# Performance work log

Hardware: AMD Instinct MI355X
Metric: run time of the kernel (lower is better)

## Reference

```python
import jax, jax.numpy as jnp
import numpy as np

D_MODEL = 1024
NUM_HEADS = 16
D_K = D_MODEL // NUM_HEADS          # 64
D_ROPE = int(D_K * 0.5)             # 32
ROPE_BASE = 10000.0


def _rope(x):
    # x: [L, B, H, D_K]; rotate first D_ROPE features, pass the rest through.
    L = x.shape[0]
    d = D_ROPE
    theta = 1.0 / (ROPE_BASE ** (jnp.arange(0, d, 2, dtype=jnp.float32) / d))  # [d/2]
    idx_theta = jnp.arange(L, dtype=jnp.float32)[:, None] * theta[None, :]     # [L, d/2]
    idx_theta2 = jnp.concatenate([idx_theta, idx_theta], axis=-1)              # [L, d]
    cos = jnp.cos(idx_theta2)[:, None, None, :].astype(x.dtype)
    sin = jnp.sin(idx_theta2)[:, None, None, :].astype(x.dtype)
    x_rope, x_pass = x[..., :d], x[..., d:]
    neg_half = jnp.concatenate([-x_rope[..., d // 2:], x_rope[..., :d // 2]], axis=-1)
    x_rope = x_rope * cos + neg_half * sin
    return jnp.concatenate([x_rope, x_pass], axis=-1)


def setup_inputs() -> dict:
    key = jax.random.key(0)
    k1, k2 = jax.random.split(key)
    L, B = 2048, 2
    x = jax.random.normal(k1, (L, B, D_MODEL), dtype=jnp.float32)
    # xavier_uniform-like init for in_proj_weight [3*d_model, d_model]
    limit = float(np.sqrt(6.0 / (3 * D_MODEL + D_MODEL)))
    in_proj_weight = jax.random.uniform(k2, (3 * D_MODEL, D_MODEL),
                                        minval=-limit, maxval=limit, dtype=jnp.float32)
    return {"x": x, "in_proj_weight": in_proj_weight}


def reference(x, in_proj_weight):
    L, B, _ = x.shape
    # fused QKV projection: [L, B, 3*d_model]
    qkv = jnp.einsum('ed,lbd->lbe', in_proj_weight, x)
    # NOTE: faithful to original quirk — reshape to per-head blocks of 3*d_k,
    # then chunk along last dim.
    qkv = qkv.reshape(L, B, NUM_HEADS, 3 * D_K)
    q, k, v = qkv[..., :D_K], qkv[..., D_K:2 * D_K], qkv[..., 2 * D_K:]
    q = _rope(q)
    k = _rope(k)
    # [L,B,H,dk] -> [H,B,L,dk]
    q, k, v = (jnp.swapaxes(t, 0, 2) for t in (q, k, v))
    scale = 1.0 / jnp.sqrt(jnp.asarray(D_K, dtype=x.dtype))
    scores = jnp.einsum('hbqd,hbkd->hbqk', q, k) * scale      # [H,B,L,L]
    attn = jax.nn.softmax(scores, axis=-1)
    out = jnp.einsum('hbqk,hbkd->hbqd', attn, v)              # [H,B,L,dk]
    out = jnp.transpose(out, (1, 2, 0, 3)).reshape(B, L, D_MODEL)
    return jnp.swapaxes(out, 0, 1)                            # [L,B,D] (batch_first falsy)
```

## Files before the change

kernel.cpp:

```cpp
#include <hip/hip_runtime.h>
#include <hip/hip_bf16.h>
#include <cstdint>
#include <cstddef>

#define L_SEQ 2048
#define BATCH 2
#define DM 1024
#define NH 16
#define DK 64
#define QKV_N 3072
#define HEAD_STRIDE 192
#define NX (4096 * 1024)
#define NW (3072 * 1024)

typedef short short8_t __attribute__((ext_vector_type(8)));
typedef short short4_t __attribute__((ext_vector_type(4)));
typedef float f32x4 __attribute__((ext_vector_type(4)));

#define MFMA32(a, b, c) __builtin_amdgcn_mfma_f32_16x16x32_bf16(a, b, c, 0, 0, 0)
#define MFMA16(a, b, c) __builtin_amdgcn_mfma_f32_16x16x16bf16_1k(a, b, c, 0, 0, 0)
#define EXP2(x) __builtin_amdgcn_exp2f(x)

static __device__ __forceinline__ unsigned pk2(float a, float b) {
  __hip_bfloat162 h = __float22bfloat162_rn(make_float2(a, b));
  union { __hip_bfloat162 h; unsigned u; } v;
  v.h = h;
  return v.u;
}

static __device__ __forceinline__ void async_copy16(const unsigned short* g,
                                                    unsigned short* l) {
  __builtin_amdgcn_global_load_lds(
      (const __attribute__((address_space(1))) unsigned int*)g,
      (__attribute__((address_space(3))) unsigned int*)l, 16, 0, 0);
}

__global__ __launch_bounds__(256) void cast_kernel(
    const float* __restrict__ X, const float* __restrict__ W,
    unsigned short* __restrict__ dst) {
  const int e = (blockIdx.x * 256 + threadIdx.x) * 8;
  const float* src = (e < NX) ? &X[e] : &W[e - NX];
  const float4 v0 = *(const float4*)src;
  const float4 v1 = *(const float4*)(src + 4);
  union { short8_t s8; unsigned u[4]; } o;
  o.u[0] = pk2(v0.x, v0.y);
  o.u[1] = pk2(v0.z, v0.w);
  o.u[2] = pk2(v1.x, v1.y);
  o.u[3] = pk2(v1.z, v1.w);
  *(short8_t*)&dst[e] = o.s8;
}

__global__ __launch_bounds__(256) void qkv_gemm_bf16(
    const unsigned short* __restrict__ Xb, const unsigned short* __restrict__ Wb,
    unsigned short* __restrict__ qkvb) {
  __shared__ __align__(16) unsigned short As[2][128 * 32];
  __shared__ __align__(16) unsigned short Bs[2][128 * 32];
  const int t = threadIdx.x;
  const int w = t >> 6;
  const int lane = t & 63;
  const int L16 = lane & 15;
  const int quad = lane >> 4;
  const int m0 = blockIdx.y * 128;
  const int n0 = blockIdx.x * 128;
  const int wm = w & 1;
  const int wn = w >> 1;

  const int c0 = w * 128 + lane;
  const int c1 = c0 + 64;
  const unsigned short* gA0 = Xb + (size_t)(m0 + (c0 >> 2)) * 1024 + (c0 & 3) * 8;
  const unsigned short* gA1 = Xb + (size_t)(m0 + (c1 >> 2)) * 1024 + (c1 & 3) * 8;
  const unsigned short* gB0 = Wb + (size_t)(n0 + (c0 >> 2)) * 1024 + (c0 & 3) * 8;
  const unsigned short* gB1 = Wb + (size_t)(n0 + (c1 >> 2)) * 1024 + (c1 & 3) * 8;

  f32x4 acc[4][4];
#pragma unroll
  for (int i = 0; i < 4; ++i)
#pragma unroll
    for (int j = 0; j < 4; ++j) acc[i][j] = (f32x4){0.f, 0.f, 0.f, 0.f};

  async_copy16(gA0, &As[0][w * 1024]);
  async_copy16(gA1, &As[0][w * 1024 + 512]);
  async_copy16(gB0, &Bs[0][w * 1024]);
  async_copy16(gB1, &Bs[0][w * 1024 + 512]);

#define GBODY(K0, BUF)                                                        \
  {                                                                           \
    __syncthreads();           \
    if ((K0) + 32 < 1024) {                                                   \
      async_copy16(gA0 + (K0) + 32, &As[(BUF) ^ 1][w * 1024]);                \
      async_copy16(gA1 + (K0) + 32, &As[(BUF) ^ 1][w * 1024 + 512]);          \
      async_copy16(gB0 + (K0) + 32, &Bs[(BUF) ^ 1][w * 1024]);                \
      async_copy16(gB1 + (K0) + 32, &Bs[(BUF) ^ 1][w * 1024 + 512]);          \
    }                                                                         \
    short8_t af[4], bfr[4];                                                   \
    _Pragma("unroll") for (int mt = 0; mt < 4; ++mt)                          \
        af[mt] = *(const short8_t*)                                           \
            &As[BUF][(wm * 64 + mt * 16 + L16) * 32 + quad * 8];              \
    _Pragma("unroll") for (int nt = 0; nt < 4; ++nt)                          \
        bfr[nt] = *(const short8_t*)                                          \
            &Bs[BUF][(wn * 64 + nt * 16 + L16) * 32 + quad * 8];              \
    _Pragma("unroll") for (int mt = 0; mt < 4; ++mt)                          \
        _Pragma("unroll") for (int nt = 0; nt < 4; ++nt)                      \
            acc[mt][nt] = MFMA32(af[mt], bfr[nt], acc[mt][nt]);               \
  }

  for (int k0 = 0; k0 < 1024; k0 += 64) {
    GBODY(k0, 0)
    GBODY(k0 + 32, 1)
  }

  const int nbase = n0 + wn * 64 + L16;
  const int chunk = (n0 >> 6) + wn;
  const int type = chunk % 3;
  if (type == 2) {
#pragma unroll
    for (int mt = 0; mt < 4; ++mt) {
      const int mbase = m0 + wm * 64 + mt * 16 + quad * 4;
#pragma unroll
      for (int reg = 0; reg < 4; ++reg) {
        const size_t r = (size_t)(mbase + reg) * QKV_N + nbase;
        const unsigned u0 = pk2(acc[mt][0][reg], acc[mt][1][reg]);
        const unsigned u1 = pk2(acc[mt][2][reg], acc[mt][3][reg]);
        qkvb[r]      = (unsigned short)u0;
        qkvb[r + 16] = (unsigned short)(u0 >> 16);
        qkvb[r + 32] = (unsigned short)u1;
        qkvb[r + 48] = (unsigned short)(u1 >> 16);
      }
    }
  } else {
    const float qs = (type == 0) ? 0.18033688011112042f : 1.0f;
    const float theta = exp2f(-(float)L16 * 0.8304820237218405f);
#pragma unroll
    for (int mt = 0; mt < 4; ++mt) {
      const int mbase = m0 + wm * 64 + mt * 16 + quad * 4;
      const int lb = mbase >> 1;
      float sv[2], cv[2];
      __sincosf((float)lb * theta, &sv[0], &cv[0]);
      __sincosf((float)(lb + 1) * theta, &sv[1], &cv[1]);
#pragma unroll
      for (int reg = 0; reg < 4; ++reg) {
        const int li = reg >> 1;
        const float v0 = acc[mt][0][reg], v1 = acc[mt][1][reg];
        const float r0 = v0 * cv[li] - v1 * sv[li];
        const float r1 = v1 * cv[li] + v0 * sv[li];
        const size_t r = (size_t)(mbase + reg) * QKV_N + nbase;
        const unsigned u0 = pk2(r0 * qs, r1 * qs);
        const unsigned u1 = pk2(acc[mt][2][reg] * qs, acc[mt][3][reg] * qs);
        qkvb[r]      = (unsigned short)u0;
        qkvb[r + 16] = (unsigned short)(u0 >> 16);
        qkvb[r + 32] = (unsigned short)u1;
        qkvb[r + 48] = (unsigned short)(u1 >> 16);
      }
    }
  }
}

__global__ __launch_bounds__(256) void attn_mfma_kernel(
    const unsigned short* __restrict__ qkvb, float* __restrict__ out) {
  __shared__ __align__(16) unsigned short Ks[2][4096];
  __shared__ __align__(16) unsigned short Vt[2][64][72];

  const int t = threadIdx.x;
  const int w = t >> 6;
  const int lane = t & 63;
  const int L16 = lane & 15;
  const int quad = lane >> 4;
  const int l0 = blockIdx.x * 128;
  const int b = blockIdx.y & 1;
  const int h = blockIdx.y >> 1;
  const int hoff = h * HEAD_STRIDE;

  const f32x4 z4 = {0.f, 0.f, 0.f, 0.f};

  short8_t bq[2][2];
#pragma unroll
  for (int mt = 0; mt < 2; ++mt)
#pragma unroll
    for (int kc = 0; kc < 2; ++kc)
      bq[mt][kc] = *(const short8_t*)
          &qkvb[((size_t)((l0 + w * 32 + mt * 16 + L16) * 2 + b)) * QKV_N +
                hoff + kc * 32 + quad * 8];

  f32x4 oc[2][4];
  float l_part[2] = {0.f, 0.f};
#pragma unroll
  for (int mt = 0; mt < 2; ++mt)
#pragma unroll
    for (int dt = 0; dt < 4; ++dt) oc[mt][dt] = z4;

  const int kr0 = w * 8 + (lane >> 3);
  const int kcs = ((lane & 7) ^ (lane >> 3)) * 8;
  const unsigned short* gK0 =
      qkvb + (size_t)(kr0 * 2 + b) * QKV_N + hoff + 64 + kcs;
  const unsigned short* gK1 = gK0 + (size_t)64 * QKV_N;
  const size_t kstep = (size_t)128 * QKV_N;

  const int vr4 = (t >> 4) * 4;
  const int vc4 = (t & 15) * 4;
  const int cgbase = vr4 >> 3;
  const int joff = vr4 & 7;
  short4_t rv[4];

#define LOAD_V(KT)                                                            \
  {                                                                           \
    const int j0 = (KT) * 64;                                                 \
    _Pragma("unroll") for (int r = 0; r < 4; ++r)                             \
        rv[r] = *(const short4_t*)&qkvb[((size_t)((j0 + vr4 + r) * 2 + b)) *  \
                                        QKV_N + hoff + 128 + vc4];            \
  }

  LOAD_V(0)
  async_copy16(gK0, &Ks[0][w * 512]);
  async_copy16(gK1, &Ks[0][w * 512 + 2048]);

  const int rsw = (L16 & 7);

#define ABODY(KT, BUF)                                                        \
  {                                                                           \
    {                                       \
      short4_t s0 = {rv[0][0], rv[1][0], rv[2][0], rv[3][0]};                 \
      short4_t s1 = {rv[0][1], rv[1][1], rv[2][1], rv[3][1]};                 \
      short4_t s2 = {rv[0][2], rv[1][2], rv[2][2], rv[3][2]};                 \
      short4_t s3 = {rv[0][3], rv[1][3], rv[2][3], rv[3][3]};                 \
      const int cg0 = (cgbase + ((vc4 >> 2) & 7)) & 7;                        \
      *(short4_t*)&Vt[BUF][vc4 + 0][cg0 * 8 + joff] = s0;                     \
      *(short4_t*)&Vt[BUF][vc4 + 1][cg0 * 8 + joff] = s1;                     \
      *(short4_t*)&Vt[BUF][vc4 + 2][cg0 * 8 + joff] = s2;                     \
      *(short4_t*)&Vt[BUF][vc4 + 3][cg0 * 8 + joff] = s3;                     \
    }                                                                         \
    __syncthreads();                                                          \
    if ((KT) + 1 < 32) {                                                      \
      async_copy16(gK0 + (size_t)((KT) + 1) * kstep, &Ks[(BUF) ^ 1][w * 512]);\
      async_copy16(gK1 + (size_t)((KT) + 1) * kstep,                          \
                   &Ks[(BUF) ^ 1][w * 512 + 2048]);                           \
      LOAD_V((KT) + 1)                                                        \
    }                                                                         \
    f32x4 sc0[4], sc1[4];                                                     \
    __builtin_amdgcn_s_setprio(1);                                            \
    _Pragma("unroll") for (int nt = 0; nt < 4; ++nt) {                        \
      const short8_t ak0 = *(const short8_t*)                                 \
          &Ks[BUF][(nt * 16 + L16) * 64 + (quad ^ rsw) * 8];                  \
      const short8_t ak1 = *(const short8_t*)                                 \
          &Ks[BUF][(nt * 16 + L16) * 64 + ((quad + 4) ^ rsw) * 8];            \
      f32x4 t0 = MFMA32(ak0, bq[0][0], z4);                                   \
      sc0[nt] = MFMA32(ak1, bq[0][1], t0);                                    \
      f32x4 t1 = MFMA32(ak0, bq[1][0], z4);                                   \
      sc1[nt] = MFMA32(ak1, bq[1][1], t1);                                    \
    }                                                                         \
    __builtin_amdgcn_s_setprio(0);                                            \
    short4_t pf[2][4];                                                        \
    _Pragma("unroll") for (int nt = 0; nt < 4; ++nt) {                        \
      float p0 = EXP2(sc0[nt][0]), p1 = EXP2(sc0[nt][1]);                     \
      float p2 = EXP2(sc0[nt][2]), p3 = EXP2(sc0[nt][3]);                     \
      l_part[0] += (p0 + p1) + (p2 + p3);                                     \
      union { short4_t s4; unsigned u[2]; } pu0;                              \
      pu0.u[0] = pk2(p0, p1);                                                 \
      pu0.u[1] = pk2(p2, p3);                                                 \
      pf[0][nt] = pu0.s4;                                                     \
      float q0 = EXP2(sc1[nt][0]), q1 = EXP2(sc1[nt][1]);                     \
      float q2 = EXP2(sc1[nt][2]), q3 = EXP2(sc1[nt][3]);                     \
      l_part[1] += (q0 + q1) + (q2 + q3);                                     \
      union { short4_t s4; unsigned u[2]; } pu1;                              \
      pu1.u[0] = pk2(q0, q1);                                                 \
      pu1.u[1] = pk2(q2, q3);                                                 \
      pf[1][nt] = pu1.s4;                                                     \
    }                                                                         \
    __builtin_amdgcn_s_setprio(1);                                            \
    _Pragma("unroll") for (int nt = 0; nt < 4; ++nt) {                        \
      _Pragma("unroll") for (int dt = 0; dt < 4; ++dt) {                      \
        const int d = dt * 16 + L16;                                          \
        const int g = 2 * nt + (quad >> 1);                                   \
        const int cg = (g + ((d >> 2) & 7)) & 7;                              \
        const short4_t vf =                                                   \
            *(const short4_t*)&Vt[BUF][d][cg * 8 + (quad & 1) * 4];           \
        oc[0][dt] = MFMA16(vf, pf[0][nt], oc[0][dt]);                         \
        oc[1][dt] = MFMA16(vf, pf[1][nt], oc[1][dt]);                         \
      }                                                                       \
    }                                                                         \
    __builtin_amdgcn_s_setprio(0);                                            \
  }

  for (int kt = 0; kt < 32; kt += 2) {
    ABODY(kt, 0)
    ABODY(kt + 1, 1)
  }

#pragma unroll
  for (int mt = 0; mt < 2; ++mt) {
    float l = l_part[mt];
    l += __shfl_xor(l, 16);
    l += __shfl_xor(l, 32);
    const float inv = 1.f / l;
    const int qrow = l0 + w * 32 + mt * 16 + L16;
    const size_t rbase = ((size_t)(qrow * 2 + b)) * DM + h * DK;
#pragma unroll
    for (int dt = 0; dt < 4; ++dt) {
      *(float4*)&out[rbase + dt * 16 + quad * 4] =
          make_float4(oc[mt][dt][0] * inv, oc[mt][dt][1] * inv,
                      oc[mt][dt][2] * inv, oc[mt][dt][3] * inv);
    }
  }
}

extern "C" void kernel_launch(void* const* d_in, const int* in_sizes, int n_in,
                              void* d_out, int out_size, void* d_ws,
                              size_t ws_size, hipStream_t stream) {
  const float* x = (const float*)d_in[0];
  const float* w = (const float*)d_in[1];
  float* out = (float*)d_out;
  unsigned short* bf = (unsigned short*)d_ws;
  unsigned short* Xb = bf;
  unsigned short* Wb = bf + NX;
  unsigned short* qkvb =
      (unsigned short*)((char*)d_ws + (16u << 20));

  cast_kernel<<<(NX + NW) / (256 * 8), 256, 0, stream>>>(x, w, bf);
  qkv_gemm_bf16<<<dim3(QKV_N / 128, (L_SEQ * BATCH) / 128), 256, 0, stream>>>(
      Xb, Wb, qkvb);
  attn_mfma_kernel<<<dim3(L_SEQ / 128, NH * BATCH), 256, 0, stream>>>(qkvb, out);
}
```

Before: 169.0 us.

## Split attention key range across two blocks and merge partial outputs

Adds a z grid dimension of size two so each attention block processes only half of the key/value sequence, writing unnormalized partial outputs and row sums. The second half's partials go to a workspace buffer that reuses the bf16 cast region. A new merge kernel adds the two partials and divides by the combined row sum. This doubles the block count to fill the GPU better and shortens each block's serial loop. In exchange it adds a kernel launch and an extra pass that reads and writes the full fp32 output.

New measurement: 180.6 us. 1.07x slower.

```diff
diff --git a/kernel.cpp b/kernel.cpp
--- a/kernel.cpp
+++ b/kernel.cpp
@@ -12,6 +12,7 @@
 #define HEAD_STRIDE 192
 #define NX (4096 * 1024)
 #define NW (3072 * 1024)
+#define NROWH (L_SEQ * BATCH * NH)
 
 typedef short short8_t __attribute__((ext_vector_type(8)));
 typedef short short4_t __attribute__((ext_vector_type(4)));
@@ -156,7 +157,8 @@
 }
 
 __global__ __launch_bounds__(256) void attn_mfma_kernel(
-    const unsigned short* __restrict__ qkvb, float* __restrict__ out) {
+    const unsigned short* __restrict__ qkvb, float* __restrict__ out,
+    float* __restrict__ part1, float* __restrict__ lsum) {
   __shared__ __align__(16) unsigned short Ks[2][4096];
   __shared__ __align__(16) unsigned short Vt[2][64][72];
 
@@ -168,6 +170,7 @@
   const int l0 = blockIdx.x * 128;
   const int b = blockIdx.y & 1;
   const int h = blockIdx.y >> 1;
+  const int z = blockIdx.z;
   const int hoff = h * HEAD_STRIDE;
 
   const f32x4 z4 = {0.f, 0.f, 0.f, 0.f};
@@ -190,20 +193,22 @@
 
   const int kr0 = w * 8 + (lane >> 3);
   const int kcs = ((lane & 7) ^ (lane >> 3)) * 8;
+  const size_t kstep = (size_t)128 * QKV_N;
   const unsigned short* gK0 =
-      qkvb + (size_t)(kr0 * 2 + b) * QKV_N + hoff + 64 + kcs;
+      qkvb + (size_t)(kr0 * 2 + b) * QKV_N + hoff + 64 + kcs +
+      (size_t)z * 16 * kstep;
   const unsigned short* gK1 = gK0 + (size_t)64 * QKV_N;
-  const size_t kstep = (size_t)128 * QKV_N;
 
   const int vr4 = (t >> 4) * 4;
   const int vc4 = (t & 15) * 4;
   const int cgbase = vr4 >> 3;
   const int joff = vr4 & 7;
+  const int vrow0 = z * 1024;
   short4_t rv[4];
 
 #define LOAD_V(KT)                                                            \
   {                                                                           \
-    const int j0 = (KT) * 64;                                                 \
+    const int j0 = (KT) * 64 + vrow0;                                         \
     _Pragma("unroll") for (int r = 0; r < 4; ++r)                             \
         rv[r] = *(const short4_t*)&qkvb[((size_t)((j0 + vr4 + r) * 2 + b)) *  \
                                         QKV_N + hoff + 128 + vc4];            \
@@ -229,7 +234,7 @@
       *(short4_t*)&Vt[BUF][vc4 + 3][cg0 * 8 + joff] = s3;                     \
     }                                                                         \
     __syncthreads();                                                          \
-    if ((KT) + 1 < 32) {                                                      \
+    if ((KT) + 1 < 16) {                                                      \
       async_copy16(gK0 + (size_t)((KT) + 1) * kstep, &Ks[(BUF) ^ 1][w * 512]);\
       async_copy16(gK1 + (size_t)((KT) + 1) * kstep,                          \
                    &Ks[(BUF) ^ 1][w * 512 + 2048]);                           \
@@ -280,26 +285,40 @@
     __builtin_amdgcn_s_setprio(0);                                            \
   }
 
-  for (int kt = 0; kt < 32; kt += 2) {
+  for (int kt = 0; kt < 16; kt += 2) {
     ABODY(kt, 0)
     ABODY(kt + 1, 1)
   }
 
+  float* const obase = (z == 0) ? out : part1;
 #pragma unroll
   for (int mt = 0; mt < 2; ++mt) {
     float l = l_part[mt];
     l += __shfl_xor(l, 16);
     l += __shfl_xor(l, 32);
-    const float inv = 1.f / l;
     const int qrow = l0 + w * 32 + mt * 16 + L16;
+    const int rowh = (qrow * 2 + b) * NH + h;
+    if (quad == 0) lsum[z * NROWH + rowh] = l;
     const size_t rbase = ((size_t)(qrow * 2 + b)) * DM + h * DK;
 #pragma unroll
     for (int dt = 0; dt < 4; ++dt) {
-      *(float4*)&out[rbase + dt * 16 + quad * 4] =
-          make_float4(oc[mt][dt][0] * inv, oc[mt][dt][1] * inv,
-                      oc[mt][dt][2] * inv, oc[mt][dt][3] * inv);
+      *(float4*)&obase[rbase + dt * 16 + quad * 4] =
+          make_float4(oc[mt][dt][0], oc[mt][dt][1],
+                      oc[mt][dt][2], oc[mt][dt][3]);
     }
   }
+}
+
+__global__ __launch_bounds__(256) void merge_kernel(
+    float* __restrict__ out, const float* __restrict__ part1,
+    const float* __restrict__ lsum) {
+  const int i = blockIdx.x * 256 + threadIdx.x;
+  const float4 a = ((const float4*)out)[i];
+  const float4 c = ((const float4*)part1)[i];
+  const int li = i >> 4;
+  const float inv = 1.f / (lsum[li] + lsum[NROWH + li]);
+  ((float4*)out)[i] = make_float4((a.x + c.x) * inv, (a.y + c.y) * inv,
+                                  (a.z + c.z) * inv, (a.w + c.w) * inv);
 }
 
 extern "C" void kernel_launch(void* const* d_in, const int* in_sizes, int n_in,
@@ -313,9 +332,14 @@
   unsigned short* Wb = bf + NX;
   unsigned short* qkvb =
       (unsigned short*)((char*)d_ws + (16u << 20));
+  float* part1 = (float*)d_ws;
+  float* lsum = (float*)((char*)d_ws + (40u << 20));
 
   cast_kernel<<<(NX + NW) / (256 * 8), 256, 0, stream>>>(x, w, bf);
   qkv_gemm_bf16<<<dim3(QKV_N / 128, (L_SEQ * BATCH) / 128), 256, 0, stream>>>(
       Xb, Wb, qkvb);
-  attn_mfma_kernel<<<dim3(L_SEQ / 128, NH * BATCH), 256, 0, stream>>>(qkvb, out);
-}
+  attn_mfma_kernel<<<dim3(L_SEQ / 128, NH * BATCH, 2), 256, 0, stream>>>(
+      qkvb, out, part1, lsum);
+  merge_kernel<<<(L_SEQ * BATCH * DM / 4) / 256, 256, 0, stream>>>(out, part1,
+                                                                   lsum);
+}
```
